# Performance work log

Measured on AMD Instinct MI355X. Metric: run time of the kernel, lower is better.

The kernel has to match this reference:

```python
import jax, jax.numpy as jnp
import numpy as np

N_NODES = 50000
N_EDGES = 600000
D = 128
H_MLP = 256
N_LABELS = 10
EPS = 0.0  # tf_geometric GIN default eps


def _gin_layer(x, src, dst, W, b):
    # gather neighbor (source) features and sum-aggregate into destinations
    msg = x[src]                                   # [E, D] irregular gather
    agg = jax.ops.segment_sum(msg, dst, num_segments=N_NODES)  # [N, D]
    h = (1.0 + EPS) * x + agg                      # GIN sum update
    return jax.nn.relu(h @ W + b)                  # dense transform + relu


def setup_inputs() -> dict:
    key = jax.random.key(0)
    ks = jax.random.split(key, 8)
    x = jax.random.normal(ks[0], (N_NODES, D), dtype=jnp.float32)
    edge_index = jax.random.randint(ks[1], (2, N_EDGES), 0, N_NODES, dtype=jnp.int32)
    s = 1.0 / np.sqrt(D)
    W0 = jax.random.normal(ks[2], (D, D), dtype=jnp.float32) * s
    W1 = jax.random.normal(ks[3], (D, D), dtype=jnp.float32) * s
    W2 = jax.random.normal(ks[4], (D, D), dtype=jnp.float32) * s
    Wm1 = jax.random.normal(ks[5], (D, H_MLP), dtype=jnp.float32) * s
    Wm2 = jax.random.normal(ks[6], (H_MLP, N_LABELS), dtype=jnp.float32) * (1.0 / np.sqrt(H_MLP))
    return {
        'x': x, 'edge_index': edge_index,
        'W0': W0, 'b0': jnp.zeros((D,), jnp.float32),
        'W1': W1, 'b1': jnp.zeros((D,), jnp.float32),
        'W2': W2, 'b2': jnp.zeros((D,), jnp.float32),
        'Wm1': Wm1, 'bm1': jnp.zeros((H_MLP,), jnp.float32),
        'Wm2': Wm2, 'bm2': jnp.zeros((N_LABELS,), jnp.float32),
    }


def reference(x, edge_index, W0, b0, W1, b1, W2, b2, Wm1, bm1, Wm2, bm2):
    src, dst = edge_index[0], edge_index[1]
    h = _gin_layer(x, src, dst, W0, b0)
    h = _gin_layer(h, src, dst, W1, b1)
    h = _gin_layer(h, src, dst, W2, b2)
    # head: Flatten is identity on [N, D]; Dense(256, relu) -> Dense(num_labels)
    h = jax.nn.relu(h @ Wm1 + bm1)
    return h @ Wm2 + bm2  # [N, num_labels] logits
```

## Files before the change

kernel.cpp:

```cpp
#include <hip/hip_runtime.h>


typedef short short8 __attribute__((ext_vector_type(8)));
typedef float v4f __attribute__((ext_vector_type(4)));
typedef float v2f __attribute__((ext_vector_type(2)));

#define BCAP 1024
#define MAXB 1024
#define NBIN 512

__device__ inline unsigned short f2bf(float f) {
  union { float f; unsigned int u; } c; c.f = f;
  unsigned int u = c.u;
  return (unsigned short)((u + 0x7fffu + ((u >> 16) & 1u)) >> 16);
}
__device__ inline float bfbits2f(unsigned int hi) {
  union { unsigned int u; float f; } c; c.u = hi; return c.f;
}
__device__ inline unsigned int pack2(float a, float b) {
  return (unsigned int)f2bf(a) | ((unsigned int)f2bf(b) << 16);
}
__device__ inline void add8(float* s, uint4 v) {
  s[0] += bfbits2f(v.x << 16); s[1] += bfbits2f(v.x & 0xffff0000u);
  s[2] += bfbits2f(v.y << 16); s[3] += bfbits2f(v.y & 0xffff0000u);
  s[4] += bfbits2f(v.z << 16); s[5] += bfbits2f(v.z & 0xffff0000u);
  s[6] += bfbits2f(v.w << 16); s[7] += bfbits2f(v.w & 0xffff0000u);
}
__device__ inline void addf8q(float* s, uint4 v) {
  v2f p;
  p = __builtin_amdgcn_cvt_pk_f32_fp8(v.x, false); s[0]  += p.x; s[1]  += p.y;
  p = __builtin_amdgcn_cvt_pk_f32_fp8(v.x, true);  s[2]  += p.x; s[3]  += p.y;
  p = __builtin_amdgcn_cvt_pk_f32_fp8(v.y, false); s[4]  += p.x; s[5]  += p.y;
  p = __builtin_amdgcn_cvt_pk_f32_fp8(v.y, true);  s[6]  += p.x; s[7]  += p.y;
  p = __builtin_amdgcn_cvt_pk_f32_fp8(v.z, false); s[8]  += p.x; s[9]  += p.y;
  p = __builtin_amdgcn_cvt_pk_f32_fp8(v.z, true);  s[10] += p.x; s[11] += p.y;
  p = __builtin_amdgcn_cvt_pk_f32_fp8(v.w, false); s[12] += p.x; s[13] += p.y;
  p = __builtin_amdgcn_cvt_pk_f32_fp8(v.w, true);  s[14] += p.x; s[15] += p.y;
}
__device__ inline unsigned char f2fp8(float v) {
  return (unsigned char)(__builtin_amdgcn_cvt_pk_fp8_f32(v, v, 0, false) & 0xff);
}
__device__ inline int wave_incl_scan_int(int v, int lane) {
#pragma unroll
  for (int off = 1; off < 64; off <<= 1) {
    int t = __shfl_up(v, off, 64);
    if (lane >= off) v += t;
  }
  return v;
}

__global__ __launch_bounds__(256) void prep_bin(
    const float* __restrict__ W0, const float* __restrict__ W1, const float* __restrict__ W2,
    const float* __restrict__ Wm1, const float* __restrict__ Wm2,
    unsigned short* __restrict__ W0T, unsigned short* __restrict__ W1T,
    unsigned short* __restrict__ W2T, unsigned short* __restrict__ Wm1T,
    unsigned short* __restrict__ Wm2T,
    const float* __restrict__ x, unsigned short* __restrict__ xb,
    unsigned char* __restrict__ xq, int n8, int PB,
    const int* __restrict__ src, const int* __restrict__ dst, int E, int per,
    int* __restrict__ bcnt, int* __restrict__ bucketA, int nbuckets) {
  __shared__ int hist[MAXB];
  __shared__ int base[MAXB];
  const int tid = threadIdx.x;
  if (blockIdx.x < PB) {
    int i = blockIdx.x * 256 + tid;
    if (i < n8) {
      const float4* p = (const float4*)x;
      float4 a = p[2 * (size_t)i], b = p[2 * (size_t)i + 1];
      uint4 o;
      o.x = pack2(a.x, a.y); o.y = pack2(a.z, a.w);
      o.z = pack2(b.x, b.y); o.w = pack2(b.z, b.w);
      ((uint4*)xb)[i] = o;
      unsigned int lo = 0, hi = 0;
      lo = __builtin_amdgcn_cvt_pk_fp8_f32(a.x, a.y, lo, false);
      lo = __builtin_amdgcn_cvt_pk_fp8_f32(a.z, a.w, lo, true);
      hi = __builtin_amdgcn_cvt_pk_fp8_f32(b.x, b.y, hi, false);
      hi = __builtin_amdgcn_cvt_pk_fp8_f32(b.z, b.w, hi, true);
      uint2 q; q.x = lo; q.y = hi;
      ((uint2*)xq)[i] = q;
    }
    if (i < 49152) {
      int w = i / 16384, r = i % 16384;
      int frag = r >> 9, l = (r >> 3) & 63, j = r & 7;
      int kq = frag >> 3, nfr = frag & 7;
      int nn = nfr * 16 + (l & 15);
      int k  = kq * 32 + (l >> 4) * 8 + j;
      const float* W = (w == 0) ? W0 : (w == 1) ? W1 : W2;
      unsigned short* O = (w == 0) ? W0T : (w == 1) ? W1T : W2T;
      O[r] = f2bf(W[k * 128 + nn]);
    } else if (i < 49152 + 32768) {
      int r = i - 49152;
      int frag = r >> 9, l = (r >> 3) & 63, j = r & 7;
      int kq = frag >> 4, nfr = frag & 15;
      int nn = nfr * 16 + (l & 15);
      int k  = kq * 32 + (l >> 4) * 8 + j;
      Wm1T[r] = f2bf(Wm1[k * 256 + nn]);
    } else if (i < 49152 + 32768 + 4096) {
      int r = i - 49152 - 32768;
      int kq = r >> 9, l = (r >> 3) & 63, j = r & 7;
      int nn = l & 15;
      int k  = kq * 32 + (l >> 4) * 8 + j;
      Wm2T[r] = (nn < 10) ? f2bf(Wm2[k * 10 + nn]) : (unsigned short)0;
    }
  } else {
    const int bb = blockIdx.x - PB;
    const int e0 = bb * per;
    const int e1 = (e0 + per < E) ? e0 + per : E;
    for (int j = tid; j < nbuckets; j += 256) hist[j] = 0;
    __syncthreads();
    for (int i = e0 + tid; i < e1; i += 256) atomicAdd(&hist[dst[i] >> 6], 1);
    __syncthreads();
    for (int j = tid; j < nbuckets; j += 256) {
      int h = hist[j];
      base[j] = h ? atomicAdd(&bcnt[j], h) : 0;
    }
    __syncthreads();
    for (int i = e0 + tid; i < e1; i += 256) {
      int d = dst[i], s = src[i];
      int b = d >> 6;
      int r = atomicAdd(&base[b], 1);
      bucketA[(size_t)b * BCAP + r] = (s << 6) | (d & 63);
    }
  }
}

__global__ __launch_bounds__(256) void fused_sort_layer(
    const unsigned short* __restrict__ Xb, const unsigned char* __restrict__ Xq,
    const int* __restrict__ bcnt, const int* __restrict__ bucketA,
    int* __restrict__ srcsS, int* __restrict__ boffs,
    const unsigned short* __restrict__ BT, const float* __restrict__ bias,
    unsigned char* __restrict__ Cq, int M) {
  __shared__ __align__(16) unsigned short As[64 * 136];
  __shared__ int rawE[BCAP];
  __shared__ int srcS[BCAP];
  __shared__ int hist[64], cur[64], offs[65];
  const int tid = threadIdx.x;
  const int lane = tid & 63;
  const int b = blockIdx.x;
  const int blk = b * 64;
  const int cnt = bcnt[b];

  for (int i = tid; i < cnt; i += 256) rawE[i] = bucketA[(size_t)b * BCAP + i];
  if (tid < 64) hist[tid] = 0;
  __syncthreads();
  for (int i = tid; i < cnt; i += 256) atomicAdd(&hist[rawE[i] & 63], 1);
  __syncthreads();
  if (tid < 64) {
    int v = hist[tid];
    int incl = wave_incl_scan_int(v, tid);
    offs[tid] = incl - v;
    cur[tid] = incl - v;
    if (tid == 63) offs[64] = incl;
  }
  __syncthreads();
  for (int i = tid; i < cnt; i += 256) {
    int e = rawE[i];
    int p = atomicAdd(&cur[e & 63], 1);
    int sv = e >> 6;
    srcS[p] = sv;
    srcsS[(size_t)b * BCAP + p] = sv;
  }
  if (tid < 65) boffs[b * 65 + tid] = offs[tid];
  __syncthreads();

  const int l = tid & 7, g = tid >> 3;
  const uint4* baseb = (const uint4*)Xb;
  const uint4* baseq = (const uint4*)Xq;
#pragma unroll
  for (int s2 = 0; s2 < 2; ++s2) {
    int nl = s2 * 32 + g;
    int node = blk + nl;
    float s[16] = {0, 0, 0, 0, 0, 0, 0, 0, 0, 0, 0, 0, 0, 0, 0, 0};
    if (node < M) {
      add8(s, baseb[(size_t)node * 16 + l * 2]);
      add8(s + 8, baseb[(size_t)node * 16 + l * 2 + 1]);
      int beg = offs[nl], c = offs[nl + 1] - beg;
      int j = 0;
      for (; j + 8 <= c; j += 8) {
        int i0 = srcS[beg + j + 0], i1 = srcS[beg + j + 1];
        int i2 = srcS[beg + j + 2], i3 = srcS[beg + j + 3];
        int i4 = srcS[beg + j + 4], i5 = srcS[beg + j + 5];
        int i6 = srcS[beg + j + 6], i7 = srcS[beg + j + 7];
        uint4 v0 = baseq[(size_t)i0 * 8 + l];
        uint4 v1 = baseq[(size_t)i1 * 8 + l];
        uint4 v2 = baseq[(size_t)i2 * 8 + l];
        uint4 v3 = baseq[(size_t)i3 * 8 + l];
        uint4 v4 = baseq[(size_t)i4 * 8 + l];
        uint4 v5 = baseq[(size_t)i5 * 8 + l];
        uint4 v6 = baseq[(size_t)i6 * 8 + l];
        uint4 v7 = baseq[(size_t)i7 * 8 + l];
        addf8q(s, v0); addf8q(s, v1); addf8q(s, v2); addf8q(s, v3);
        addf8q(s, v4); addf8q(s, v5); addf8q(s, v6); addf8q(s, v7);
      }
      if (j + 4 <= c) {
        int i0 = srcS[beg + j + 0], i1 = srcS[beg + j + 1];
        int i2 = srcS[beg + j + 2], i3 = srcS[beg + j + 3];
        uint4 v0 = baseq[(size_t)i0 * 8 + l];
        uint4 v1 = baseq[(size_t)i1 * 8 + l];
        uint4 v2 = baseq[(size_t)i2 * 8 + l];
        uint4 v3 = baseq[(size_t)i3 * 8 + l];
        addf8q(s, v0); addf8q(s, v1); addf8q(s, v2); addf8q(s, v3);
        j += 4;
      }
      if (j + 2 <= c) {
        int i0 = srcS[beg + j + 0], i1 = srcS[beg + j + 1];
        uint4 v0 = baseq[(size_t)i0 * 8 + l];
        uint4 v1 = baseq[(size_t)i1 * 8 + l];
        addf8q(s, v0); addf8q(s, v1);
        j += 2;
      }
      if (j < c) addf8q(s, baseq[(size_t)srcS[beg + j] * 8 + l]);
    }
    uint4 o0, o1;
    o0.x = pack2(s[0], s[1]);   o0.y = pack2(s[2], s[3]);
    o0.z = pack2(s[4], s[5]);   o0.w = pack2(s[6], s[7]);
    o1.x = pack2(s[8], s[9]);   o1.y = pack2(s[10], s[11]);
    o1.z = pack2(s[12], s[13]); o1.w = pack2(s[14], s[15]);
    *(uint4*)&As[nl * 136 + l * 16] = o0;
    *(uint4*)&As[nl * 136 + l * 16 + 8] = o1;
  }
  __syncthreads();

  const int w = tid >> 6;
  const int wm = w & 1, wn = w >> 1;
  const int l15 = lane & 15, quad = lane >> 4;
  const int mb = wm * 32, nb2 = wn * 64;

  v4f acc[2][4];
#pragma unroll
  for (int mf = 0; mf < 2; ++mf)
#pragma unroll
    for (int nf = 0; nf < 4; ++nf) acc[mf][nf] = (v4f)0.f;

#pragma unroll
  for (int k0 = 0; k0 < 128; k0 += 32) {
    const int kq = k0 >> 5;
    short8 a[2], bv[4];
#pragma unroll
    for (int mf = 0; mf < 2; ++mf)
      a[mf] = *(const short8*)&As[(mb + mf * 16 + l15) * 136 + k0 + quad * 8];
#pragma unroll
    for (int nf = 0; nf < 4; ++nf)
      bv[nf] = *(const short8*)(BT + (size_t)(kq * 8 + wn * 4 + nf) * 512 + lane * 8);
#pragma unroll
    for (int mf = 0; mf < 2; ++mf)
#pragma unroll
      for (int nf = 0; nf < 4; ++nf)
        acc[mf][nf] = __builtin_amdgcn_mfma_f32_16x16x32_bf16(a[mf], bv[nf], acc[mf][nf], 0, 0, 0);
  }
  __syncthreads();

  unsigned char* Cs = (unsigned char*)As;
#pragma unroll
  for (int mf = 0; mf < 2; ++mf)
#pragma unroll
    for (int r = 0; r < 4; ++r) {
      int row = mb + mf * 16 + quad * 4 + r;
#pragma unroll
      for (int nf = 0; nf < 4; ++nf) {
        int col = nb2 + nf * 16 + l15;
        Cs[row * 128 + col] = f2fp8(fmaxf(acc[mf][nf][r] + bias[col], 0.f));
      }
    }
  __syncthreads();
  uint4* dst4 = (uint4*)(Cq + (size_t)blk * 128);
  const uint4* s4 = (const uint4*)Cs;
  if (blk + 64 <= M) {
    dst4[tid] = s4[tid];
    dst4[tid + 256] = s4[tid + 256];
  } else {
    for (int c2 = tid; c2 < 512; c2 += 256)
      if (blk + (c2 >> 3) < M) dst4[c2] = s4[c2];
  }
}

__global__ __launch_bounds__(256) void fused_layer(
    const unsigned char* __restrict__ Xq,
    const int* __restrict__ bcnt,
    const int* __restrict__ srcsS, const int* __restrict__ boffs,
    const unsigned short* __restrict__ BT, const float* __restrict__ bias,
    unsigned char* __restrict__ Cq, int M) {
  __shared__ __align__(16) unsigned short As[64 * 136];
  __shared__ int srcS[BCAP];
  __shared__ int offs[65];
  const int tid = threadIdx.x;
  const int lane = tid & 63;
  const int b = blockIdx.x;
  const int blk = b * 64;
  const int cnt = bcnt[b];

  if (tid < 65) offs[tid] = boffs[b * 65 + tid];
  for (int i = tid; i < cnt; i += 256) srcS[i] = srcsS[(size_t)b * BCAP + i];
  __syncthreads();

  const int l = tid & 7, g = tid >> 3;
  const uint4* baseq = (const uint4*)Xq;
#pragma unroll
  for (int s2 = 0; s2 < 2; ++s2) {
    int nl = s2 * 32 + g;
    int node = blk + nl;
    float s[16] = {0, 0, 0, 0, 0, 0, 0, 0, 0, 0, 0, 0, 0, 0, 0, 0};
    if (node < M) {
      addf8q(s, baseq[(size_t)node * 8 + l]);
      int beg = offs[nl], c = offs[nl + 1] - beg;
      int j = 0;
      for (; j + 8 <= c; j += 8) {
        int i0 = srcS[beg + j + 0], i1 = srcS[beg + j + 1];
        int i2 = srcS[beg + j + 2], i3 = srcS[beg + j + 3];
        int i4 = srcS[beg + j + 4], i5 = srcS[beg + j + 5];
        int i6 = srcS[beg + j + 6], i7 = srcS[beg + j + 7];
        uint4 v0 = baseq[(size_t)i0 * 8 + l];
        uint4 v1 = baseq[(size_t)i1 * 8 + l];
        uint4 v2 = baseq[(size_t)i2 * 8 + l];
        uint4 v3 = baseq[(size_t)i3 * 8 + l];
        uint4 v4 = baseq[(size_t)i4 * 8 + l];
        uint4 v5 = baseq[(size_t)i5 * 8 + l];
        uint4 v6 = baseq[(size_t)i6 * 8 + l];
        uint4 v7 = baseq[(size_t)i7 * 8 + l];
        addf8q(s, v0); addf8q(s, v1); addf8q(s, v2); addf8q(s, v3);
        addf8q(s, v4); addf8q(s, v5); addf8q(s, v6); addf8q(s, v7);
      }
      if (j + 4 <= c) {
        int i0 = srcS[beg + j + 0], i1 = srcS[beg + j + 1];
        int i2 = srcS[beg + j + 2], i3 = srcS[beg + j + 3];
        uint4 v0 = baseq[(size_t)i0 * 8 + l];
        uint4 v1 = baseq[(size_t)i1 * 8 + l];
        uint4 v2 = baseq[(size_t)i2 * 8 + l];
        uint4 v3 = baseq[(size_t)i3 * 8 + l];
        addf8q(s, v0); addf8q(s, v1); addf8q(s, v2); addf8q(s, v3);
        j += 4;
      }
      if (j + 2 <= c) {
        int i0 = srcS[beg + j + 0], i1 = srcS[beg + j + 1];
        uint4 v0 = baseq[(size_t)i0 * 8 + l];
        uint4 v1 = baseq[(size_t)i1 * 8 + l];
        addf8q(s, v0); addf8q(s, v1);
        j += 2;
      }
      if (j < c) addf8q(s, baseq[(size_t)srcS[beg + j] * 8 + l]);
    }
    uint4 o0, o1;
    o0.x = pack2(s[0], s[1]);   o0.y = pack2(s[2], s[3]);
    o0.z = pack2(s[4], s[5]);   o0.w = pack2(s[6], s[7]);
    o1.x = pack2(s[8], s[9]);   o1.y = pack2(s[10], s[11]);
    o1.z = pack2(s[12], s[13]); o1.w = pack2(s[14], s[15]);
    *(uint4*)&As[nl * 136 + l * 16] = o0;
    *(uint4*)&As[nl * 136 + l * 16 + 8] = o1;
  }
  __syncthreads();

  const int w = tid >> 6;
  const int wm = w & 1, wn = w >> 1;
  const int l15 = lane & 15, quad = lane >> 4;
  const int mb = wm * 32, nb2 = wn * 64;

  v4f acc[2][4];
#pragma unroll
  for (int mf = 0; mf < 2; ++mf)
#pragma unroll
    for (int nf = 0; nf < 4; ++nf) acc[mf][nf] = (v4f)0.f;

#pragma unroll
  for (int k0 = 0; k0 < 128; k0 += 32) {
    const int kq = k0 >> 5;
    short8 a[2], bv[4];
#pragma unroll
    for (int mf = 0; mf < 2; ++mf)
      a[mf] = *(const short8*)&As[(mb + mf * 16 + l15) * 136 + k0 + quad * 8];
#pragma unroll
    for (int nf = 0; nf < 4; ++nf)
      bv[nf] = *(const short8*)(BT + (size_t)(kq * 8 + wn * 4 + nf) * 512 + lane * 8);
#pragma unroll
    for (int mf = 0; mf < 2; ++mf)
#pragma unroll
      for (int nf = 0; nf < 4; ++nf)
        acc[mf][nf] = __builtin_amdgcn_mfma_f32_16x16x32_bf16(a[mf], bv[nf], acc[mf][nf], 0, 0, 0);
  }
  __syncthreads();

  unsigned char* Cs = (unsigned char*)As;
#pragma unroll
  for (int mf = 0; mf < 2; ++mf)
#pragma unroll
    for (int r = 0; r < 4; ++r) {
      int row = mb + mf * 16 + quad * 4 + r;
#pragma unroll
      for (int nf = 0; nf < 4; ++nf) {
        int col = nb2 + nf * 16 + l15;
        Cs[row * 128 + col] = f2fp8(fmaxf(acc[mf][nf][r] + bias[col], 0.f));
      }
    }
  __syncthreads();
  uint4* dst4 = (uint4*)(Cq + (size_t)blk * 128);
  const uint4* s4 = (const uint4*)Cs;
  if (blk + 64 <= M) {
    dst4[tid] = s4[tid];
    dst4[tid + 256] = s4[tid + 256];
  } else {
    for (int c2 = tid; c2 < 512; c2 += 256)
      if (blk + (c2 >> 3) < M) dst4[c2] = s4[c2];
  }
}

__global__ __launch_bounds__(256) void fused_l3_head(
    const unsigned char* __restrict__ Xq,
    const int* __restrict__ bcnt,
    const int* __restrict__ srcsS, const int* __restrict__ boffs,
    const unsigned short* __restrict__ W2T, const float* __restrict__ b2,
    const unsigned short* __restrict__ Wm1T, const float* __restrict__ bm1,
    const unsigned short* __restrict__ Wm2T, const float* __restrict__ bm2,
    float* __restrict__ out, int M, int NOUT) {
  __shared__ __align__(16) unsigned char lds[64 * 264 * 2];
  unsigned short* As = (unsigned short*)lds;
  int* srcS = (int*)(lds + 64 * 136 * 2);
  unsigned short* Hs = (unsigned short*)lds;
  __shared__ int offs[65];
  const int tid = threadIdx.x;
  const int lane = tid & 63;
  const int b = blockIdx.x;
  const int blk = b * 64;
  const int cnt = bcnt[b];

  if (tid < 65) offs[tid] = boffs[b * 65 + tid];
  for (int i = tid; i < cnt; i += 256) srcS[i] = srcsS[(size_t)b * BCAP + i];
  __syncthreads();

  const int l = tid & 7, g = tid >> 3;
  const uint4* baseq = (const uint4*)Xq;
#pragma unroll
  for (int s2 = 0; s2 < 2; ++s2) {
    int nl = s2 * 32 + g;
    int node = blk + nl;
    float s[16] = {0, 0, 0, 0, 0, 0, 0, 0, 0, 0, 0, 0, 0, 0, 0, 0};
    if (node < M) {
      addf8q(s, baseq[(size_t)node * 8 + l]);
      int beg = offs[nl], c = offs[nl + 1] - beg;
      int j = 0;
      for (; j + 8 <= c; j += 8) {
        int i0 = srcS[beg + j + 0], i1 = srcS[beg + j + 1];
        int i2 = srcS[beg + j + 2], i3 = srcS[beg + j + 3];
        int i4 = srcS[beg + j + 4], i5 = srcS[beg + j + 5];
        int i6 = srcS[beg + j + 6], i7 = srcS[beg + j + 7];
        uint4 v0 = baseq[(size_t)i0 * 8 + l];
        uint4 v1 = baseq[(size_t)i1 * 8 + l];
        uint4 v2 = baseq[(size_t)i2 * 8 + l];
        uint4 v3 = baseq[(size_t)i3 * 8 + l];
        uint4 v4 = baseq[(size_t)i4 * 8 + l];
        uint4 v5 = baseq[(size_t)i5 * 8 + l];
        uint4 v6 = baseq[(size_t)i6 * 8 + l];
        uint4 v7 = baseq[(size_t)i7 * 8 + l];
        addf8q(s, v0); addf8q(s, v1); addf8q(s, v2); addf8q(s, v3);
        addf8q(s, v4); addf8q(s, v5); addf8q(s, v6); addf8q(s, v7);
      }
      if (j + 4 <= c) {
        int i0 = srcS[beg + j + 0], i1 = srcS[beg + j + 1];
        int i2 = srcS[beg + j + 2], i3 = srcS[beg + j + 3];
        uint4 v0 = baseq[(size_t)i0 * 8 + l];
        uint4 v1 = baseq[(size_t)i1 * 8 + l];
        uint4 v2 = baseq[(size_t)i2 * 8 + l];
        uint4 v3 = baseq[(size_t)i3 * 8 + l];
        addf8q(s, v0); addf8q(s, v1); addf8q(s, v2); addf8q(s, v3);
        j += 4;
      }
      if (j + 2 <= c) {
        int i0 = srcS[beg + j + 0], i1 = srcS[beg + j + 1];
        uint4 v0 = baseq[(size_t)i0 * 8 + l];
        uint4 v1 = baseq[(size_t)i1 * 8 + l];
        addf8q(s, v0); addf8q(s, v1);
        j += 2;
      }
      if (j < c) addf8q(s, baseq[(size_t)srcS[beg + j] * 8 + l]);
    }
    uint4 o0, o1;
    o0.x = pack2(s[0], s[1]);   o0.y = pack2(s[2], s[3]);
    o0.z = pack2(s[4], s[5]);   o0.w = pack2(s[6], s[7]);
    o1.x = pack2(s[8], s[9]);   o1.y = pack2(s[10], s[11]);
    o1.z = pack2(s[12], s[13]); o1.w = pack2(s[14], s[15]);
    *(uint4*)&As[nl * 136 + l * 16] = o0;
    *(uint4*)&As[nl * 136 + l * 16 + 8] = o1;
  }
  __syncthreads();

  const int w = tid >> 6;
  const int wm = w & 1, wn = w >> 1;
  const int l15 = lane & 15, quad = lane >> 4;
  const int mb = wm * 32, nb2 = wn * 64;

  v4f acc[2][4];
#pragma unroll
  for (int mf = 0; mf < 2; ++mf)
#pragma unroll
    for (int nf = 0; nf < 4; ++nf) acc[mf][nf] = (v4f)0.f;

#pragma unroll
  for (int k0 = 0; k0 < 128; k0 += 32) {
    const int kq = k0 >> 5;
    short8 a[2], bv[4];
#pragma unroll
    for (int mf = 0; mf < 2; ++mf)
      a[mf] = *(const short8*)&As[(mb + mf * 16 + l15) * 136 + k0 + quad * 8];
#pragma unroll
    for (int nf = 0; nf < 4; ++nf)
      bv[nf] = *(const short8*)(W2T + (size_t)(kq * 8 + wn * 4 + nf) * 512 + lane * 8);
#pragma unroll
    for (int mf = 0; mf < 2; ++mf)
#pragma unroll
      for (int nf = 0; nf < 4; ++nf)
        acc[mf][nf] = __builtin_amdgcn_mfma_f32_16x16x32_bf16(a[mf], bv[nf], acc[mf][nf], 0, 0, 0);
  }
  __syncthreads();

#pragma unroll
  for (int mf = 0; mf < 2; ++mf)
#pragma unroll
    for (int r = 0; r < 4; ++r) {
      int row = mb + mf * 16 + quad * 4 + r;
#pragma unroll
      for (int nf = 0; nf < 4; ++nf) {
        int col = nb2 + nf * 16 + l15;
        As[row * 136 + col] = f2bf(fmaxf(acc[mf][nf][r] + b2[col], 0.f));
      }
    }
  __syncthreads();

  const int nbH = wn * 128;
  v4f acc2[2][8];
#pragma unroll
  for (int mf = 0; mf < 2; ++mf)
#pragma unroll
    for (int nf = 0; nf < 8; ++nf) acc2[mf][nf] = (v4f)0.f;

#pragma unroll
  for (int k0 = 0; k0 < 128; k0 += 32) {
    const int kq = k0 >> 5;
    short8 a[2];
#pragma unroll
    for (int mf = 0; mf < 2; ++mf)
      a[mf] = *(const short8*)&As[(mb + mf * 16 + l15) * 136 + k0 + quad * 8];
#pragma unroll
    for (int nf = 0; nf < 8; ++nf) {
      short8 bb = *(const short8*)(Wm1T + (size_t)(kq * 16 + wn * 8 + nf) * 512 + lane * 8);
#pragma unroll
      for (int mf = 0; mf < 2; ++mf)
        acc2[mf][nf] = __builtin_amdgcn_mfma_f32_16x16x32_bf16(a[mf], bb, acc2[mf][nf], 0, 0, 0);
    }
  }
  __syncthreads();

#pragma unroll
  for (int mf = 0; mf < 2; ++mf)
#pragma unroll
    for (int r = 0; r < 4; ++r) {
      int row = mb + mf * 16 + quad * 4 + r;
#pragma unroll
      for (int nf = 0; nf < 8; ++nf) {
        int col = nbH + nf * 16 + l15;
        Hs[row * 264 + col] = f2bf(fmaxf(acc2[mf][nf][r] + bm1[col], 0.f));
      }
    }
  __syncthreads();

  const int rowl = w * 16 + l15;
  v4f acc3 = (v4f)0.f;
#pragma unroll
  for (int k0 = 0; k0 < 256; k0 += 32)
    acc3 = __builtin_amdgcn_mfma_f32_16x16x32_bf16(
        *(const short8*)&Hs[rowl * 264 + k0 + quad * 8],
        *(const short8*)(Wm2T + (size_t)(k0 >> 5) * 512 + lane * 8), acc3, 0, 0, 0);
  float bb = (l15 < NOUT) ? bm2[l15] : 0.f;
#pragma unroll
  for (int r = 0; r < 4; ++r) {
    int grow = blk + w * 16 + quad * 4 + r;
    if (grow < M && l15 < NOUT) out[(size_t)grow * NOUT + l15] = acc3[r] + bb;
  }
}


extern "C" void kernel_launch(void* const* d_in, const int* in_sizes, int n_in,
                              void* d_out, int out_size, void* d_ws, size_t ws_size,
                              hipStream_t stream) {
  const float* x   = (const float*)d_in[0];
  const int*   ei  = (const int*)d_in[1];
  const float* W0  = (const float*)d_in[2];
  const float* b0  = (const float*)d_in[3];
  const float* W1  = (const float*)d_in[4];
  const float* b1  = (const float*)d_in[5];
  const float* W2  = (const float*)d_in[6];
  const float* b2  = (const float*)d_in[7];
  const float* Wm1 = (const float*)d_in[8];
  const float* bm1 = (const float*)d_in[9];
  const float* Wm2 = (const float*)d_in[10];
  const float* bm2 = (const float*)d_in[11];
  float* out = (float*)d_out;

  const int D = 128;
  const int N = in_sizes[0] / D;
  const int E = in_sizes[1] / 2;
  const int L = in_sizes[11];
  const int nb = (N + 63) / 64;

  const int* srcv = ei;
  const int* dstv = ei + E;

  char* ws = (char*)d_ws;
  size_t off = 0;
  auto alloc = [&](size_t bytes) -> void* {
    void* p = ws + off;
    off = (off + bytes + 255) & ~(size_t)255;
    return p;
  };
  int* bcnt    = (int*)alloc((size_t)MAXB * 4);
  int* bucketA = (int*)alloc((size_t)nb * BCAP * 4);
  int* srcsS   = (int*)alloc((size_t)nb * BCAP * 4);
  int* boffs   = (int*)alloc((size_t)nb * 65 * 4);
  unsigned short* xb   = (unsigned short*)alloc((size_t)N * 128 * 2);
  unsigned char*  xq   = (unsigned char*)alloc((size_t)N * 128);
  unsigned char*  h1q  = (unsigned char*)alloc((size_t)N * 128);
  unsigned char*  h2q  = (unsigned char*)alloc((size_t)N * 128);
  unsigned short* W0T  = (unsigned short*)alloc(128 * 128 * 2);
  unsigned short* W1T  = (unsigned short*)alloc(128 * 128 * 2);
  unsigned short* W2T  = (unsigned short*)alloc(128 * 128 * 2);
  unsigned short* Wm1T = (unsigned short*)alloc(256 * 128 * 2);
  unsigned short* Wm2T = (unsigned short*)alloc(16 * 256 * 2);
  (void)ws_size; (void)n_in; (void)out_size;

  const int tpb = 256;
  int n8 = N * 16;
  const int PB = (n8 + tpb - 1) / tpb;
  int per = (E + NBIN - 1) / NBIN;

  hipMemsetAsync(bcnt, 0, (size_t)MAXB * 4, stream);
  prep_bin<<<dim3(PB + NBIN), dim3(tpb), 0, stream>>>(
      W0, W1, W2, Wm1, Wm2, W0T, W1T, W2T, Wm1T, Wm2T,
      x, xb, xq, n8, PB, srcv, dstv, E, per, bcnt, bucketA, nb);

  dim3 lgrid(nb);
  fused_sort_layer<<<lgrid, dim3(tpb), 0, stream>>>(
      xb, xq, bcnt, bucketA, srcsS, boffs, W0T, b0, h1q, N);
  fused_layer<<<lgrid, dim3(tpb), 0, stream>>>(
      h1q, bcnt, srcsS, boffs, W1T, b1, h2q, N);
  fused_l3_head<<<lgrid, dim3(tpb), 0, stream>>>(
      h2q, bcnt, srcsS, boffs, W2T, b2, Wm1T, bm1, Wm2T, bm2, out, N, L);
}
```

Before: 198.6 us.

## Convert fused GIN layer kernels to persistent blocks with atomic tile scheduling

The three fused layer kernels now launch a fixed grid of 512 blocks. Each block repeatedly takes the next 64-node tile from a global atomic counter instead of mapping one tile to each block. The intent is to balance the irregular per-tile edge counts dynamically and to cut block launch overhead across the 782 tiles. In exchange it adds an atomic and two barriers per tile, and it relies on the memset covering the counters placed right after bcnt.

```diff
diff --git a/kernel.cpp b/kernel.cpp
--- a/kernel.cpp
+++ b/kernel.cpp
@@ -8,6 +8,7 @@
 #define BCAP 1024
 #define MAXB 1024
 #define NBIN 512
+#define LGRID 512
 
 __device__ inline unsigned short f2bf(float f) {
   union { float f; unsigned int u; } c; c.f = f;
@@ -129,148 +130,156 @@
     const int* __restrict__ bcnt, const int* __restrict__ bucketA,
     int* __restrict__ srcsS, int* __restrict__ boffs,
     const unsigned short* __restrict__ BT, const float* __restrict__ bias,
-    unsigned char* __restrict__ Cq, int M) {
+    unsigned char* __restrict__ Cq, int M, int nb, int* __restrict__ ctr) {
   __shared__ __align__(16) unsigned short As[64 * 136];
   __shared__ int rawE[BCAP];
   __shared__ int srcS[BCAP];
   __shared__ int hist[64], cur[64], offs[65];
+  __shared__ int sb;
   const int tid = threadIdx.x;
   const int lane = tid & 63;
-  const int b = blockIdx.x;
-  const int blk = b * 64;
-  const int cnt = bcnt[b];
-
-  for (int i = tid; i < cnt; i += 256) rawE[i] = bucketA[(size_t)b * BCAP + i];
-  if (tid < 64) hist[tid] = 0;
-  __syncthreads();
-  for (int i = tid; i < cnt; i += 256) atomicAdd(&hist[rawE[i] & 63], 1);
-  __syncthreads();
-  if (tid < 64) {
-    int v = hist[tid];
-    int incl = wave_incl_scan_int(v, tid);
-    offs[tid] = incl - v;
-    cur[tid] = incl - v;
-    if (tid == 63) offs[64] = incl;
-  }
-  __syncthreads();
-  for (int i = tid; i < cnt; i += 256) {
-    int e = rawE[i];
-    int p = atomicAdd(&cur[e & 63], 1);
-    int sv = e >> 6;
-    srcS[p] = sv;
-    srcsS[(size_t)b * BCAP + p] = sv;
-  }
-  if (tid < 65) boffs[b * 65 + tid] = offs[tid];
-  __syncthreads();
-
-  const int l = tid & 7, g = tid >> 3;
-  const uint4* baseb = (const uint4*)Xb;
-  const uint4* baseq = (const uint4*)Xq;
-#pragma unroll
-  for (int s2 = 0; s2 < 2; ++s2) {
-    int nl = s2 * 32 + g;
-    int node = blk + nl;
-    float s[16] = {0, 0, 0, 0, 0, 0, 0, 0, 0, 0, 0, 0, 0, 0, 0, 0};
-    if (node < M) {
-      add8(s, baseb[(size_t)node * 16 + l * 2]);
-      add8(s + 8, baseb[(size_t)node * 16 + l * 2 + 1]);
-      int beg = offs[nl], c = offs[nl + 1] - beg;
-      int j = 0;
-      for (; j + 8 <= c; j += 8) {
-        int i0 = srcS[beg + j + 0], i1 = srcS[beg + j + 1];
-        int i2 = srcS[beg + j + 2], i3 = srcS[beg + j + 3];
-        int i4 = srcS[beg + j + 4], i5 = srcS[beg + j + 5];
-        int i6 = srcS[beg + j + 6], i7 = srcS[beg + j + 7];
-        uint4 v0 = baseq[(size_t)i0 * 8 + l];
-        uint4 v1 = baseq[(size_t)i1 * 8 + l];
-        uint4 v2 = baseq[(size_t)i2 * 8 + l];
-        uint4 v3 = baseq[(size_t)i3 * 8 + l];
-        uint4 v4 = baseq[(size_t)i4 * 8 + l];
-        uint4 v5 = baseq[(size_t)i5 * 8 + l];
-        uint4 v6 = baseq[(size_t)i6 * 8 + l];
-        uint4 v7 = baseq[(size_t)i7 * 8 + l];
-        addf8q(s, v0); addf8q(s, v1); addf8q(s, v2); addf8q(s, v3);
-        addf8q(s, v4); addf8q(s, v5); addf8q(s, v6); addf8q(s, v7);
-      }
-      if (j + 4 <= c) {
-        int i0 = srcS[beg + j + 0], i1 = srcS[beg + j + 1];
-        int i2 = srcS[beg + j + 2], i3 = srcS[beg + j + 3];
-        uint4 v0 = baseq[(size_t)i0 * 8 + l];
-        uint4 v1 = baseq[(size_t)i1 * 8 + l];
-        uint4 v2 = baseq[(size_t)i2 * 8 + l];
-        uint4 v3 = baseq[(size_t)i3 * 8 + l];
-        addf8q(s, v0); addf8q(s, v1); addf8q(s, v2); addf8q(s, v3);
-        j += 4;
-      }
-      if (j + 2 <= c) {
-        int i0 = srcS[beg + j + 0], i1 = srcS[beg + j + 1];
-        uint4 v0 = baseq[(size_t)i0 * 8 + l];
-        uint4 v1 = baseq[(size_t)i1 * 8 + l];
-        addf8q(s, v0); addf8q(s, v1);
-        j += 2;
-      }
-      if (j < c) addf8q(s, baseq[(size_t)srcS[beg + j] * 8 + l]);
-    }
-    uint4 o0, o1;
-    o0.x = pack2(s[0], s[1]);   o0.y = pack2(s[2], s[3]);
-    o0.z = pack2(s[4], s[5]);   o0.w = pack2(s[6], s[7]);
-    o1.x = pack2(s[8], s[9]);   o1.y = pack2(s[10], s[11]);
-    o1.z = pack2(s[12], s[13]); o1.w = pack2(s[14], s[15]);
-    *(uint4*)&As[nl * 136 + l * 16] = o0;
-    *(uint4*)&As[nl * 136 + l * 16 + 8] = o1;
-  }
-  __syncthreads();
-
-  const int w = tid >> 6;
-  const int wm = w & 1, wn = w >> 1;
-  const int l15 = lane & 15, quad = lane >> 4;
-  const int mb = wm * 32, nb2 = wn * 64;
-
-  v4f acc[2][4];
-#pragma unroll
-  for (int mf = 0; mf < 2; ++mf)
-#pragma unroll
-    for (int nf = 0; nf < 4; ++nf) acc[mf][nf] = (v4f)0.f;
-
-#pragma unroll
-  for (int k0 = 0; k0 < 128; k0 += 32) {
-    const int kq = k0 >> 5;
-    short8 a[2], bv[4];
-#pragma unroll
-    for (int mf = 0; mf < 2; ++mf)
-      a[mf] = *(const short8*)&As[(mb + mf * 16 + l15) * 136 + k0 + quad * 8];
-#pragma unroll
-    for (int nf = 0; nf < 4; ++nf)
-      bv[nf] = *(const short8*)(BT + (size_t)(kq * 8 + wn * 4 + nf) * 512 + lane * 8);
-#pragma unroll
-    for (int mf = 0; mf < 2; ++mf)
+
+  for (;;) {
+    __syncthreads();
+    if (tid == 0) sb = atomicAdd(ctr, 1);
+    __syncthreads();
+    const int b = sb;
+    if (b >= nb) break;
+    const int blk = b * 64;
+    const int cnt = bcnt[b];
+
+    for (int i = tid; i < cnt; i += 256) rawE[i] = bucketA[(size_t)b * BCAP + i];
+    if (tid < 64) hist[tid] = 0;
+    __syncthreads();
+    for (int i = tid; i < cnt; i += 256) atomicAdd(&hist[rawE[i] & 63], 1);
+    __syncthreads();
+    if (tid < 64) {
+      int v = hist[tid];
+      int incl = wave_incl_scan_int(v, tid);
+      offs[tid] = incl - v;
+      cur[tid] = incl - v;
+      if (tid == 63) offs[64] = incl;
+    }
+    __syncthreads();
+    for (int i = tid; i < cnt; i += 256) {
+      int e = rawE[i];
+      int p = atomicAdd(&cur[e & 63], 1);
+      int sv = e >> 6;
+      srcS[p] = sv;
+      srcsS[(size_t)b * BCAP + p] = sv;
+    }
+    if (tid < 65) boffs[b * 65 + tid] = offs[tid];
+    __syncthreads();
+
+    const int l = tid & 7, g = tid >> 3;
+    const uint4* baseb = (const uint4*)Xb;
+    const uint4* baseq = (const uint4*)Xq;
+#pragma unroll
+    for (int s2 = 0; s2 < 2; ++s2) {
+      int nl = s2 * 32 + g;
+      int node = blk + nl;
+      float s[16] = {0, 0, 0, 0, 0, 0, 0, 0, 0, 0, 0, 0, 0, 0, 0, 0};
+      if (node < M) {
+        add8(s, baseb[(size_t)node * 16 + l * 2]);
+        add8(s + 8, baseb[(size_t)node * 16 + l * 2 + 1]);
+        int beg = offs[nl], c = offs[nl + 1] - beg;
+        int j = 0;
+        for (; j + 8 <= c; j += 8) {
+          int i0 = srcS[beg + j + 0], i1 = srcS[beg + j + 1];
+          int i2 = srcS[beg + j + 2], i3 = srcS[beg + j + 3];
+          int i4 = srcS[beg + j + 4], i5 = srcS[beg + j + 5];
+          int i6 = srcS[beg + j + 6], i7 = srcS[beg + j + 7];
+          uint4 v0 = baseq[(size_t)i0 * 8 + l];
+          uint4 v1 = baseq[(size_t)i1 * 8 + l];
+          uint4 v2 = baseq[(size_t)i2 * 8 + l];
+          uint4 v3 = baseq[(size_t)i3 * 8 + l];
+          uint4 v4 = baseq[(size_t)i4 * 8 + l];
+          uint4 v5 = baseq[(size_t)i5 * 8 + l];
+          uint4 v6 = baseq[(size_t)i6 * 8 + l];
+          uint4 v7 = baseq[(size_t)i7 * 8 + l];
+          addf8q(s, v0); addf8q(s, v1); addf8q(s, v2); addf8q(s, v3);
+          addf8q(s, v4); addf8q(s, v5); addf8q(s, v6); addf8q(s, v7);
+        }
+        if (j + 4 <= c) {
+          int i0 = srcS[beg + j + 0], i1 = srcS[beg + j + 1];
+          int i2 = srcS[beg + j + 2], i3 = srcS[beg + j + 3];
+          uint4 v0 = baseq[(size_t)i0 * 8 + l];
+          uint4 v1 = baseq[(size_t)i1 * 8 + l];
+          uint4 v2 = baseq[(size_t)i2 * 8 + l];
+          uint4 v3 = baseq[(size_t)i3 * 8 + l];
+          addf8q(s, v0); addf8q(s, v1); addf8q(s, v2); addf8q(s, v3);
+          j += 4;
+        }
+        if (j + 2 <= c) {
+          int i0 = srcS[beg + j + 0], i1 = srcS[beg + j + 1];
+          uint4 v0 = baseq[(size_t)i0 * 8 + l];
+          uint4 v1 = baseq[(size_t)i1 * 8 + l];
+          addf8q(s, v0); addf8q(s, v1);
+          j += 2;
+        }
+        if (j < c) addf8q(s, baseq[(size_t)srcS[beg + j] * 8 + l]);
+      }
+      uint4 o0, o1;
+      o0.x = pack2(s[0], s[1]);   o0.y = pack2(s[2], s[3]);
+      o0.z = pack2(s[4], s[5]);   o0.w = pack2(s[6], s[7]);
+      o1.x = pack2(s[8], s[9]);   o1.y = pack2(s[10], s[11]);
+      o1.z = pack2(s[12], s[13]); o1.w = pack2(s[14], s[15]);
+      *(uint4*)&As[nl * 136 + l * 16] = o0;
+      *(uint4*)&As[nl * 136 + l * 16 + 8] = o1;
+    }
+    __syncthreads();
+
+    const int w = tid >> 6;
+    const int wm = w & 1, wn = w >> 1;
+    const int l15 = lane & 15, quad = lane >> 4;
+    const int mb = wm * 32, nb2 = wn * 64;
+
+    v4f acc[2][4];
+#pragma unroll
+    for (int mf = 0; mf < 2; ++mf)
+#pragma unroll
+      for (int nf = 0; nf < 4; ++nf) acc[mf][nf] = (v4f)0.f;
+
+#pragma unroll
+    for (int k0 = 0; k0 < 128; k0 += 32) {
+      const int kq = k0 >> 5;
+      short8 a[2], bv[4];
+#pragma unroll
+      for (int mf = 0; mf < 2; ++mf)
+        a[mf] = *(const short8*)&As[(mb + mf * 16 + l15) * 136 + k0 + quad * 8];
 #pragma unroll
       for (int nf = 0; nf < 4; ++nf)
-        acc[mf][nf] = __builtin_amdgcn_mfma_f32_16x16x32_bf16(a[mf], bv[nf], acc[mf][nf], 0, 0, 0);
-  }
-  __syncthreads();
-
-  unsigned char* Cs = (unsigned char*)As;
-#pragma unroll
-  for (int mf = 0; mf < 2; ++mf)
-#pragma unroll
-    for (int r = 0; r < 4; ++r) {
-      int row = mb + mf * 16 + quad * 4 + r;
-#pragma unroll
-      for (int nf = 0; nf < 4; ++nf) {
-        int col = nb2 + nf * 16 + l15;
-        Cs[row * 128 + col] = f2fp8(fmaxf(acc[mf][nf][r] + bias[col], 0.f));
-      }
-    }
-  __syncthreads();
-  uint4* dst4 = (uint4*)(Cq + (size_t)blk * 128);
-  const uint4* s4 = (const uint4*)Cs;
-  if (blk + 64 <= M) {
-    dst4[tid] = s4[tid];
-    dst4[tid + 256] = s4[tid + 256];
-  } else {
-    for (int c2 = tid; c2 < 512; c2 += 256)
-      if (blk + (c2 >> 3) < M) dst4[c2] = s4[c2];
+        bv[nf] = *(const short8*)(BT + (size_t)(kq * 8 + wn * 4 + nf) * 512 + lane * 8);
+#pragma unroll
+      for (int mf = 0; mf < 2; ++mf)
+#pragma unroll
+        for (int nf = 0; nf < 4; ++nf)
+          acc[mf][nf] = __builtin_amdgcn_mfma_f32_16x16x32_bf16(a[mf], bv[nf], acc[mf][nf], 0, 0, 0);
+    }
+    __syncthreads();
+
+    unsigned char* Cs = (unsigned char*)As;
+#pragma unroll
+    for (int mf = 0; mf < 2; ++mf)
+#pragma unroll
+      for (int r = 0; r < 4; ++r) {
+        int row = mb + mf * 16 + quad * 4 + r;
+#pragma unroll
+        for (int nf = 0; nf < 4; ++nf) {
+          int col = nb2 + nf * 16 + l15;
+          Cs[row * 128 + col] = f2fp8(fmaxf(acc[mf][nf][r] + bias[col], 0.f));
+        }
+      }
+    __syncthreads();
+    uint4* dst4 = (uint4*)(Cq + (size_t)blk * 128);
+    const uint4* s4 = (const uint4*)Cs;
+    if (blk + 64 <= M) {
+      dst4[tid] = s4[tid];
+      dst4[tid + 256] = s4[tid + 256];
+    } else {
+      for (int c2 = tid; c2 < 512; c2 += 256)
+        if (blk + (c2 >> 3) < M) dst4[c2] = s4[c2];
+    }
   }
 }
 
@@ -279,126 +288,134 @@
     const int* __restrict__ bcnt,
     const int* __restrict__ srcsS, const int* __restrict__ boffs,
     const unsigned short* __restrict__ BT, const float* __restrict__ bias,
-    unsigned char* __restrict__ Cq, int M) {
+    unsigned char* __restrict__ Cq, int M, int nb, int* __restrict__ ctr) {
   __shared__ __align__(16) unsigned short As[64 * 136];
   __shared__ int srcS[BCAP];
   __shared__ int offs[65];
+  __shared__ int sb;
   const int tid = threadIdx.x;
   const int lane = tid & 63;
-  const int b = blockIdx.x;
-  const int blk = b * 64;
-  const int cnt = bcnt[b];
-
-  if (tid < 65) offs[tid] = boffs[b * 65 + tid];
-  for (int i = tid; i < cnt; i += 256) srcS[i] = srcsS[(size_t)b * BCAP + i];
-  __syncthreads();
-
-  const int l = tid & 7, g = tid >> 3;
-  const uint4* baseq = (const uint4*)Xq;
-#pragma unroll
-  for (int s2 = 0; s2 < 2; ++s2) {
-    int nl = s2 * 32 + g;
-    int node = blk + nl;
-    float s[16] = {0, 0, 0, 0, 0, 0, 0, 0, 0, 0, 0, 0, 0, 0, 0, 0};
-    if (node < M) {
-      addf8q(s, baseq[(size_t)node * 8 + l]);
-      int beg = offs[nl], c = offs[nl + 1] - beg;
-      int j = 0;
-      for (; j + 8 <= c; j += 8) {
-        int i0 = srcS[beg + j + 0], i1 = srcS[beg + j + 1];
-        int i2 = srcS[beg + j + 2], i3 = srcS[beg + j + 3];
-        int i4 = srcS[beg + j + 4], i5 = srcS[beg + j + 5];
-        int i6 = srcS[beg + j + 6], i7 = srcS[beg + j + 7];
-        uint4 v0 = baseq[(size_t)i0 * 8 + l];
-        uint4 v1 = baseq[(size_t)i1 * 8 + l];
-        uint4 v2 = baseq[(size_t)i2 * 8 + l];
-        uint4 v3 = baseq[(size_t)i3 * 8 + l];
-        uint4 v4 = baseq[(size_t)i4 * 8 + l];
-        uint4 v5 = baseq[(size_t)i5 * 8 + l];
-        uint4 v6 = baseq[(size_t)i6 * 8 + l];
-        uint4 v7 = baseq[(size_t)i7 * 8 + l];
-        addf8q(s, v0); addf8q(s, v1); addf8q(s, v2); addf8q(s, v3);
-        addf8q(s, v4); addf8q(s, v5); addf8q(s, v6); addf8q(s, v7);
-      }
-      if (j + 4 <= c) {
-        int i0 = srcS[beg + j + 0], i1 = srcS[beg + j + 1];
-        int i2 = srcS[beg + j + 2], i3 = srcS[beg + j + 3];
-        uint4 v0 = baseq[(size_t)i0 * 8 + l];
-        uint4 v1 = baseq[(size_t)i1 * 8 + l];
-        uint4 v2 = baseq[(size_t)i2 * 8 + l];
-        uint4 v3 = baseq[(size_t)i3 * 8 + l];
-        addf8q(s, v0); addf8q(s, v1); addf8q(s, v2); addf8q(s, v3);
-        j += 4;
-      }
-      if (j + 2 <= c) {
-        int i0 = srcS[beg + j + 0], i1 = srcS[beg + j + 1];
-        uint4 v0 = baseq[(size_t)i0 * 8 + l];
-        uint4 v1 = baseq[(size_t)i1 * 8 + l];
-        addf8q(s, v0); addf8q(s, v1);
-        j += 2;
-      }
-      if (j < c) addf8q(s, baseq[(size_t)srcS[beg + j] * 8 + l]);
-    }
-    uint4 o0, o1;
-    o0.x = pack2(s[0], s[1]);   o0.y = pack2(s[2], s[3]);
-    o0.z = pack2(s[4], s[5]);   o0.w = pack2(s[6], s[7]);
-    o1.x = pack2(s[8], s[9]);   o1.y = pack2(s[10], s[11]);
-    o1.z = pack2(s[12], s[13]); o1.w = pack2(s[14], s[15]);
-    *(uint4*)&As[nl * 136 + l * 16] = o0;
-    *(uint4*)&As[nl * 136 + l * 16 + 8] = o1;
-  }
-  __syncthreads();
-
-  const int w = tid >> 6;
-  const int wm = w & 1, wn = w >> 1;
-  const int l15 = lane & 15, quad = lane >> 4;
-  const int mb = wm * 32, nb2 = wn * 64;
-
-  v4f acc[2][4];
-#pragma unroll
-  for (int mf = 0; mf < 2; ++mf)
-#pragma unroll
-    for (int nf = 0; nf < 4; ++nf) acc[mf][nf] = (v4f)0.f;
-
-#pragma unroll
-  for (int k0 = 0; k0 < 128; k0 += 32) {
-    const int kq = k0 >> 5;
-    short8 a[2], bv[4];
-#pragma unroll
-    for (int mf = 0; mf < 2; ++mf)
-      a[mf] = *(const short8*)&As[(mb + mf * 16 + l15) * 136 + k0 + quad * 8];
-#pragma unroll
-    for (int nf = 0; nf < 4; ++nf)
-      bv[nf] = *(const short8*)(BT + (size_t)(kq * 8 + wn * 4 + nf) * 512 + lane * 8);
-#pragma unroll
-    for (int mf = 0; mf < 2; ++mf)
+
+  for (;;) {
+    __syncthreads();
+    if (tid == 0) sb = atomicAdd(ctr, 1);
+    __syncthreads();
+    const int b = sb;
+    if (b >= nb) break;
+    const int blk = b * 64;
+    const int cnt = bcnt[b];
+
+    if (tid < 65) offs[tid] = boffs[b * 65 + tid];
+    for (int i = tid; i < cnt; i += 256) srcS[i] = srcsS[(size_t)b * BCAP + i];
+    __syncthreads();
+
+    const int l = tid & 7, g = tid >> 3;
+    const uint4* baseq = (const uint4*)Xq;
+#pragma unroll
+    for (int s2 = 0; s2 < 2; ++s2) {
+      int nl = s2 * 32 + g;
+      int node = blk + nl;
+      float s[16] = {0, 0, 0, 0, 0, 0, 0, 0, 0, 0, 0, 0, 0, 0, 0, 0};
+      if (node < M) {
+        addf8q(s, baseq[(size_t)node * 8 + l]);
+        int beg = offs[nl], c = offs[nl + 1] - beg;
+        int j = 0;
+        for (; j + 8 <= c; j += 8) {
+          int i0 = srcS[beg + j + 0], i1 = srcS[beg + j + 1];
+          int i2 = srcS[beg + j + 2], i3 = srcS[beg + j + 3];
+          int i4 = srcS[beg + j + 4], i5 = srcS[beg + j + 5];
+          int i6 = srcS[beg + j + 6], i7 = srcS[beg + j + 7];
+          uint4 v0 = baseq[(size_t)i0 * 8 + l];
+          uint4 v1 = baseq[(size_t)i1 * 8 + l];
+          uint4 v2 = baseq[(size_t)i2 * 8 + l];
+          uint4 v3 = baseq[(size_t)i3 * 8 + l];
+          uint4 v4 = baseq[(size_t)i4 * 8 + l];
+          uint4 v5 = baseq[(size_t)i5 * 8 + l];
+          uint4 v6 = baseq[(size_t)i6 * 8 + l];
+          uint4 v7 = baseq[(size_t)i7 * 8 + l];
+          addf8q(s, v0); addf8q(s, v1); addf8q(s, v2); addf8q(s, v3);
+          addf8q(s, v4); addf8q(s, v5); addf8q(s, v6); addf8q(s, v7);
+        }
+        if (j + 4 <= c) {
+          int i0 = srcS[beg + j + 0], i1 = srcS[beg + j + 1];
+          int i2 = srcS[beg + j + 2], i3 = srcS[beg + j + 3];
+          uint4 v0 = baseq[(size_t)i0 * 8 + l];
+          uint4 v1 = baseq[(size_t)i1 * 8 + l];
+          uint4 v2 = baseq[(size_t)i2 * 8 + l];
+          uint4 v3 = baseq[(size_t)i3 * 8 + l];
+          addf8q(s, v0); addf8q(s, v1); addf8q(s, v2); addf8q(s, v3);
+          j += 4;
+        }
+        if (j + 2 <= c) {
+          int i0 = srcS[beg + j + 0], i1 = srcS[beg + j + 1];
+          uint4 v0 = baseq[(size_t)i0 * 8 + l];
+          uint4 v1 = baseq[(size_t)i1 * 8 + l];
+          addf8q(s, v0); addf8q(s, v1);
+          j += 2;
+        }
+        if (j < c) addf8q(s, baseq[(size_t)srcS[beg + j] * 8 + l]);
+      }
+      uint4 o0, o1;
+      o0.x = pack2(s[0], s[1]);   o0.y = pack2(s[2], s[3]);
+      o0.z = pack2(s[4], s[5]);   o0.w = pack2(s[6], s[7]);
+      o1.x = pack2(s[8], s[9]);   o1.y = pack2(s[10], s[11]);
+      o1.z = pack2(s[12], s[13]); o1.w = pack2(s[14], s[15]);
+      *(uint4*)&As[nl * 136 + l * 16] = o0;
+      *(uint4*)&As[nl * 136 + l * 16 + 8] = o1;
+    }
+    __syncthreads();
+
+    const int w = tid >> 6;
+    const int wm = w & 1, wn = w >> 1;
+    const int l15 = lane & 15, quad = lane >> 4;
+    const int mb = wm * 32, nb2 = wn * 64;
+
+    v4f acc[2][4];
+#pragma unroll
+    for (int mf = 0; mf < 2; ++mf)
+#pragma unroll
+      for (int nf = 0; nf < 4; ++nf) acc[mf][nf] = (v4f)0.f;
+
+#pragma unroll
+    for (int k0 = 0; k0 < 128; k0 += 32) {
+      const int kq = k0 >> 5;
+      short8 a[2], bv[4];
+#pragma unroll
+      for (int mf = 0; mf < 2; ++mf)
+        a[mf] = *(const short8*)&As[(mb + mf * 16 + l15) * 136 + k0 + quad * 8];
 #pragma unroll
       for (int nf = 0; nf < 4; ++nf)
-        acc[mf][nf] = __builtin_amdgcn_mfma_f32_16x16x32_bf16(a[mf], bv[nf], acc[mf][nf], 0, 0, 0);
-  }
-  __syncthreads();
-
-  unsigned char* Cs = (unsigned char*)As;
-#pragma unroll
-  for (int mf = 0; mf < 2; ++mf)
-#pragma unroll
-    for (int r = 0; r < 4; ++r) {
-      int row = mb + mf * 16 + quad * 4 + r;
-#pragma unroll
-      for (int nf = 0; nf < 4; ++nf) {
-        int col = nb2 + nf * 16 + l15;
-        Cs[row * 128 + col] = f2fp8(fmaxf(acc[mf][nf][r] + bias[col], 0.f));
-      }
-    }
-  __syncthreads();
-  uint4* dst4 = (uint4*)(Cq + (size_t)blk * 128);
-  const uint4* s4 = (const uint4*)Cs;
-  if (blk + 64 <= M) {
-    dst4[tid] = s4[tid];
-    dst4[tid + 256] = s4[tid + 256];
-  } else {
-    for (int c2 = tid; c2 < 512; c2 += 256)
-      if (blk + (c2 >> 3) < M) dst4[c2] = s4[c2];
+        bv[nf] = *(const short8*)(BT + (size_t)(kq * 8 + wn * 4 + nf) * 512 + lane * 8);
+#pragma unroll
+      for (int mf = 0; mf < 2; ++mf)
+#pragma unroll
+        for (int nf = 0; nf < 4; ++nf)
+          acc[mf][nf] = __builtin_amdgcn_mfma_f32_16x16x32_bf16(a[mf], bv[nf], acc[mf][nf], 0, 0, 0);
+    }
+    __syncthreads();
+
+    unsigned char* Cs = (unsigned char*)As;
+#pragma unroll
+    for (int mf = 0; mf < 2; ++mf)
+#pragma unroll
+      for (int r = 0; r < 4; ++r) {
+        int row = mb + mf * 16 + quad * 4 + r;
+#pragma unroll
+        for (int nf = 0; nf < 4; ++nf) {
+          int col = nb2 + nf * 16 + l15;
+          Cs[row * 128 + col] = f2fp8(fmaxf(acc[mf][nf][r] + bias[col], 0.f));
+        }
+      }
+    __syncthreads();
+    uint4* dst4 = (uint4*)(Cq + (size_t)blk * 128);
+    const uint4* s4 = (const uint4*)Cs;
+    if (blk + 64 <= M) {
+      dst4[tid] = s4[tid];
+      dst4[tid + 256] = s4[tid + 256];
+    } else {
+      for (int c2 = tid; c2 < 512; c2 += 256)
+        if (blk + (c2 >> 3) < M) dst4[c2] = s4[c2];
+    }
   }
 }
 
@@ -409,169 +426,177 @@
     const unsigned short* __restrict__ W2T, const float* __restrict__ b2,
     const unsigned short* __restrict__ Wm1T, const float* __restrict__ bm1,
     const unsigned short* __restrict__ Wm2T, const float* __restrict__ bm2,
-    float* __restrict__ out, int M, int NOUT) {
+    float* __restrict__ out, int M, int NOUT, int nb, int* __restrict__ ctr) {
   __shared__ __align__(16) unsigned char lds[64 * 264 * 2];
   unsigned short* As = (unsigned short*)lds;
   int* srcS = (int*)(lds + 64 * 136 * 2);
   unsigned short* Hs = (unsigned short*)lds;
   __shared__ int offs[65];
+  __shared__ int sb;
   const int tid = threadIdx.x;
   const int lane = tid & 63;
-  const int b = blockIdx.x;
-  const int blk = b * 64;
-  const int cnt = bcnt[b];
-
-  if (tid < 65) offs[tid] = boffs[b * 65 + tid];
-  for (int i = tid; i < cnt; i += 256) srcS[i] = srcsS[(size_t)b * BCAP + i];
-  __syncthreads();
-
-  const int l = tid & 7, g = tid >> 3;
-  const uint4* baseq = (const uint4*)Xq;
-#pragma unroll
-  for (int s2 = 0; s2 < 2; ++s2) {
-    int nl = s2 * 32 + g;
-    int node = blk + nl;
-    float s[16] = {0, 0, 0, 0, 0, 0, 0, 0, 0, 0, 0, 0, 0, 0, 0, 0};
-    if (node < M) {
-      addf8q(s, baseq[(size_t)node * 8 + l]);
-      int beg = offs[nl], c = offs[nl + 1] - beg;
-      int j = 0;
-      for (; j + 8 <= c; j += 8) {
-        int i0 = srcS[beg + j + 0], i1 = srcS[beg + j + 1];
-        int i2 = srcS[beg + j + 2], i3 = srcS[beg + j + 3];
-        int i4 = srcS[beg + j + 4], i5 = srcS[beg + j + 5];
-        int i6 = srcS[beg + j + 6], i7 = srcS[beg + j + 7];
-        uint4 v0 = baseq[(size_t)i0 * 8 + l];
-        uint4 v1 = baseq[(size_t)i1 * 8 + l];
-        uint4 v2 = baseq[(size_t)i2 * 8 + l];
-        uint4 v3 = baseq[(size_t)i3 * 8 + l];
-        uint4 v4 = baseq[(size_t)i4 * 8 + l];
-        uint4 v5 = baseq[(size_t)i5 * 8 + l];
-        uint4 v6 = baseq[(size_t)i6 * 8 + l];
-        uint4 v7 = baseq[(size_t)i7 * 8 + l];
-        addf8q(s, v0); addf8q(s, v1); addf8q(s, v2); addf8q(s, v3);
-        addf8q(s, v4); addf8q(s, v5); addf8q(s, v6); addf8q(s, v7);
-      }
-      if (j + 4 <= c) {
-        int i0 = srcS[beg + j + 0], i1 = srcS[beg + j + 1];
-        int i2 = srcS[beg + j + 2], i3 = srcS[beg + j + 3];
-        uint4 v0 = baseq[(size_t)i0 * 8 + l];
-        uint4 v1 = baseq[(size_t)i1 * 8 + l];
-        uint4 v2 = baseq[(size_t)i2 * 8 + l];
-        uint4 v3 = baseq[(size_t)i3 * 8 + l];
-        addf8q(s, v0); addf8q(s, v1); addf8q(s, v2); addf8q(s, v3);
-        j += 4;
-      }
-      if (j + 2 <= c) {
-        int i0 = srcS[beg + j + 0], i1 = srcS[beg + j + 1];
-        uint4 v0 = baseq[(size_t)i0 * 8 + l];
-        uint4 v1 = baseq[(size_t)i1 * 8 + l];
-        addf8q(s, v0); addf8q(s, v1);
-        j += 2;
-      }
-      if (j < c) addf8q(s, baseq[(size_t)srcS[beg + j] * 8 + l]);
-    }
-    uint4 o0, o1;
-    o0.x = pack2(s[0], s[1]);   o0.y = pack2(s[2], s[3]);
-    o0.z = pack2(s[4], s[5]);   o0.w = pack2(s[6], s[7]);
-    o1.x = pack2(s[8], s[9]);   o1.y = pack2(s[10], s[11]);
-    o1.z = pack2(s[12], s[13]); o1.w = pack2(s[14], s[15]);
-    *(uint4*)&As[nl * 136 + l * 16] = o0;
-    *(uint4*)&As[nl * 136 + l * 16 + 8] = o1;
-  }
-  __syncthreads();
-
-  const int w = tid >> 6;
-  const int wm = w & 1, wn = w >> 1;
-  const int l15 = lane & 15, quad = lane >> 4;
-  const int mb = wm * 32, nb2 = wn * 64;
-
-  v4f acc[2][4];
-#pragma unroll
-  for (int mf = 0; mf < 2; ++mf)
-#pragma unroll
-    for (int nf = 0; nf < 4; ++nf) acc[mf][nf] = (v4f)0.f;
-
-#pragma unroll
-  for (int k0 = 0; k0 < 128; k0 += 32) {
-    const int kq = k0 >> 5;
-    short8 a[2], bv[4];
-#pragma unroll
-    for (int mf = 0; mf < 2; ++mf)
-      a[mf] = *(const short8*)&As[(mb + mf * 16 + l15) * 136 + k0 + quad * 8];
-#pragma unroll
-    for (int nf = 0; nf < 4; ++nf)
-      bv[nf] = *(const short8*)(W2T + (size_t)(kq * 8 + wn * 4 + nf) * 512 + lane * 8);
-#pragma unroll
-    for (int mf = 0; mf < 2; ++mf)
+
+  for (;;) {
+    __syncthreads();
+    if (tid == 0) sb = atomicAdd(ctr, 1);
+    __syncthreads();
+    const int b = sb;
+    if (b >= nb) break;
+    const int blk = b * 64;
+    const int cnt = bcnt[b];
+
+    if (tid < 65) offs[tid] = boffs[b * 65 + tid];
+    for (int i = tid; i < cnt; i += 256) srcS[i] = srcsS[(size_t)b * BCAP + i];
+    __syncthreads();
+
+    const int l = tid & 7, g = tid >> 3;
+    const uint4* baseq = (const uint4*)Xq;
+#pragma unroll
+    for (int s2 = 0; s2 < 2; ++s2) {
+      int nl = s2 * 32 + g;
+      int node = blk + nl;
+      float s[16] = {0, 0, 0, 0, 0, 0, 0, 0, 0, 0, 0, 0, 0, 0, 0, 0};
+      if (node < M) {
+        addf8q(s, baseq[(size_t)node * 8 + l]);
+        int beg = offs[nl], c = offs[nl + 1] - beg;
+        int j = 0;
+        for (; j + 8 <= c; j += 8) {
+          int i0 = srcS[beg + j + 0], i1 = srcS[beg + j + 1];
+          int i2 = srcS[beg + j + 2], i3 = srcS[beg + j + 3];
+          int i4 = srcS[beg + j + 4], i5 = srcS[beg + j + 5];
+          int i6 = srcS[beg + j + 6], i7 = srcS[beg + j + 7];
+          uint4 v0 = baseq[(size_t)i0 * 8 + l];
+          uint4 v1 = baseq[(size_t)i1 * 8 + l];
+          uint4 v2 = baseq[(size_t)i2 * 8 + l];
+          uint4 v3 = baseq[(size_t)i3 * 8 + l];
+          uint4 v4 = baseq[(size_t)i4 * 8 + l];
+          uint4 v5 = baseq[(size_t)i5 * 8 + l];
+          uint4 v6 = baseq[(size_t)i6 * 8 + l];
+          uint4 v7 = baseq[(size_t)i7 * 8 + l];
+          addf8q(s, v0); addf8q(s, v1); addf8q(s, v2); addf8q(s, v3);
+          addf8q(s, v4); addf8q(s, v5); addf8q(s, v6); addf8q(s, v7);
+        }
+        if (j + 4 <= c) {
+          int i0 = srcS[beg + j + 0], i1 = srcS[beg + j + 1];
+          int i2 = srcS[beg + j + 2], i3 = srcS[beg + j + 3];
+          uint4 v0 = baseq[(size_t)i0 * 8 + l];
+          uint4 v1 = baseq[(size_t)i1 * 8 + l];
+          uint4 v2 = baseq[(size_t)i2 * 8 + l];
+          uint4 v3 = baseq[(size_t)i3 * 8 + l];
+          addf8q(s, v0); addf8q(s, v1); addf8q(s, v2); addf8q(s, v3);
+          j += 4;
+        }
+        if (j + 2 <= c) {
+          int i0 = srcS[beg + j + 0], i1 = srcS[beg + j + 1];
+          uint4 v0 = baseq[(size_t)i0 * 8 + l];
+          uint4 v1 = baseq[(size_t)i1 * 8 + l];
+          addf8q(s, v0); addf8q(s, v1);
+          j += 2;
+        }
+        if (j < c) addf8q(s, baseq[(size_t)srcS[beg + j] * 8 + l]);
+      }
+      uint4 o0, o1;
+      o0.x = pack2(s[0], s[1]);   o0.y = pack2(s[2], s[3]);
+      o0.z = pack2(s[4], s[5]);   o0.w = pack2(s[6], s[7]);
+      o1.x = pack2(s[8], s[9]);   o1.y = pack2(s[10], s[11]);
+      o1.z = pack2(s[12], s[13]); o1.w = pack2(s[14], s[15]);
+      *(uint4*)&As[nl * 136 + l * 16] = o0;
+      *(uint4*)&As[nl * 136 + l * 16 + 8] = o1;
+    }
+    __syncthreads();
+
+    const int w = tid >> 6;
+    const int wm = w & 1, wn = w >> 1;
+    const int l15 = lane & 15, quad = lane >> 4;
+    const int mb = wm * 32, nb2 = wn * 64;
+
+    v4f acc[2][4];
+#pragma unroll
+    for (int mf = 0; mf < 2; ++mf)
+#pragma unroll
+      for (int nf = 0; nf < 4; ++nf) acc[mf][nf] = (v4f)0.f;
+
+#pragma unroll
+    for (int k0 = 0; k0 < 128; k0 += 32) {
+      const int kq = k0 >> 5;
+      short8 a[2], bv[4];
+#pragma unroll
+      for (int mf = 0; mf < 2; ++mf)
+        a[mf] = *(const short8*)&As[(mb + mf * 16 + l15) * 136 + k0 + quad * 8];
 #pragma unroll
       for (int nf = 0; nf < 4; ++nf)
-        acc[mf][nf] = __builtin_amdgcn_mfma_f32_16x16x32_bf16(a[mf], bv[nf], acc[mf][nf], 0, 0, 0);
-  }
-  __syncthreads();
-
-#pragma unroll
-  for (int mf = 0; mf < 2; ++mf)
+        bv[nf] = *(const short8*)(W2T + (size_t)(kq * 8 + wn * 4 + nf) * 512 + lane * 8);
+#pragma unroll
+      for (int mf = 0; mf < 2; ++mf)
+#pragma unroll
+        for (int nf = 0; nf < 4; ++nf)
+          acc[mf][nf] = __builtin_amdgcn_mfma_f32_16x16x32_bf16(a[mf], bv[nf], acc[mf][nf], 0, 0, 0);
+    }
+    __syncthreads();
+
+#pragma unroll
+    for (int mf = 0; mf < 2; ++mf)
+#pragma unroll
+      for (int r = 0; r < 4; ++r) {
+        int row = mb + mf * 16 + quad * 4 + r;
+#pragma unroll
+        for (int nf = 0; nf < 4; ++nf) {
+          int col = nb2 + nf * 16 + l15;
+          As[row * 136 + col] = f2bf(fmaxf(acc[mf][nf][r] + b2[col], 0.f));
+        }
+      }
+    __syncthreads();
+
+    const int nbH = wn * 128;
+    v4f acc2[2][8];
+#pragma unroll
+    for (int mf = 0; mf < 2; ++mf)
+#pragma unroll
+      for (int nf = 0; nf < 8; ++nf) acc2[mf][nf] = (v4f)0.f;
+
+#pragma unroll
+    for (int k0 = 0; k0 < 128; k0 += 32) {
+      const int kq = k0 >> 5;
+      short8 a[2];
+#pragma unroll
+      for (int mf = 0; mf < 2; ++mf)
+        a[mf] = *(const short8*)&As[(mb + mf * 16 + l15) * 136 + k0 + quad * 8];
+#pragma unroll
+      for (int nf = 0; nf < 8; ++nf) {
+        short8 bb = *(const short8*)(Wm1T + (size_t)(kq * 16 + wn * 8 + nf) * 512 + lane * 8);
+#pragma unroll
+        for (int mf = 0; mf < 2; ++mf)
+          acc2[mf][nf] = __builtin_amdgcn_mfma_f32_16x16x32_bf16(a[mf], bb, acc2[mf][nf], 0, 0, 0);
+      }
+    }
+    __syncthreads();
+
+#pragma unroll
+    for (int mf = 0; mf < 2; ++mf)
+#pragma unroll
+      for (int r = 0; r < 4; ++r) {
+        int row = mb + mf * 16 + quad * 4 + r;
+#pragma unroll
+        for (int nf = 0; nf < 8; ++nf) {
+          int col = nbH + nf * 16 + l15;
+          Hs[row * 264 + col] = f2bf(fmaxf(acc2[mf][nf][r] + bm1[col], 0.f));
+        }
+      }
+    __syncthreads();
+
+    const int rowl = w * 16 + l15;
+    v4f acc3 = (v4f)0.f;
+#pragma unroll
+    for (int k0 = 0; k0 < 256; k0 += 32)
+      acc3 = __builtin_amdgcn_mfma_f32_16x16x32_bf16(
+          *(const short8*)&Hs[rowl * 264 + k0 + quad * 8],
+          *(const short8*)(Wm2T + (size_t)(k0 >> 5) * 512 + lane * 8), acc3, 0, 0, 0);
+    float bb = (l15 < NOUT) ? bm2[l15] : 0.f;
 #pragma unroll
     for (int r = 0; r < 4; ++r) {
-      int row = mb + mf * 16 + quad * 4 + r;
-#pragma unroll
-      for (int nf = 0; nf < 4; ++nf) {
-        int col = nb2 + nf * 16 + l15;
-        As[row * 136 + col] = f2bf(fmaxf(acc[mf][nf][r] + b2[col], 0.f));
-      }
-    }
-  __syncthreads();
-
-  const int nbH = wn * 128;
-  v4f acc2[2][8];
-#pragma unroll
-  for (int mf = 0; mf < 2; ++mf)
-#pragma unroll
-    for (int nf = 0; nf < 8; ++nf) acc2[mf][nf] = (v4f)0.f;
-
-#pragma unroll
-  for (int k0 = 0; k0 < 128; k0 += 32) {
-    const int kq = k0 >> 5;
-    short8 a[2];
-#pragma unroll
-    for (int mf = 0; mf < 2; ++mf)
-      a[mf] = *(const short8*)&As[(mb + mf * 16 + l15) * 136 + k0 + quad * 8];
-#pragma unroll
-    for (int nf = 0; nf < 8; ++nf) {
-      short8 bb = *(const short8*)(Wm1T + (size_t)(kq * 16 + wn * 8 + nf) * 512 + lane * 8);
-#pragma unroll
-      for (int mf = 0; mf < 2; ++mf)
-        acc2[mf][nf] = __builtin_amdgcn_mfma_f32_16x16x32_bf16(a[mf], bb, acc2[mf][nf], 0, 0, 0);
-    }
-  }
-  __syncthreads();
-
-#pragma unroll
-  for (int mf = 0; mf < 2; ++mf)
-#pragma unroll
-    for (int r = 0; r < 4; ++r) {
-      int row = mb + mf * 16 + quad * 4 + r;
-#pragma unroll
-      for (int nf = 0; nf < 8; ++nf) {
-        int col = nbH + nf * 16 + l15;
-        Hs[row * 264 + col] = f2bf(fmaxf(acc2[mf][nf][r] + bm1[col], 0.f));
-      }
-    }
-  __syncthreads();
-
-  const int rowl = w * 16 + l15;
-  v4f acc3 = (v4f)0.f;
-#pragma unroll
-  for (int k0 = 0; k0 < 256; k0 += 32)
-    acc3 = __builtin_amdgcn_mfma_f32_16x16x32_bf16(
-        *(const short8*)&Hs[rowl * 264 + k0 + quad * 8],
-        *(const short8*)(Wm2T + (size_t)(k0 >> 5) * 512 + lane * 8), acc3, 0, 0, 0);
-  float bb = (l15 < NOUT) ? bm2[l15] : 0.f;
-#pragma unroll
-  for (int r = 0; r < 4; ++r) {
-    int grow = blk + w * 16 + quad * 4 + r;
-    if (grow < M && l15 < NOUT) out[(size_t)grow * NOUT + l15] = acc3[r] + bb;
+      int grow = blk + w * 16 + quad * 4 + r;
+      if (grow < M && l15 < NOUT) out[(size_t)grow * NOUT + l15] = acc3[r] + bb;
+    }
   }
 }
 
@@ -610,6 +635,7 @@
     return p;
   };
   int* bcnt    = (int*)alloc((size_t)MAXB * 4);
+  int* ctrs    = (int*)alloc(256);
   int* bucketA = (int*)alloc((size_t)nb * BCAP * 4);
   int* srcsS   = (int*)alloc((size_t)nb * BCAP * 4);
   int* boffs   = (int*)alloc((size_t)nb * 65 * 4);
@@ -629,16 +655,17 @@
   const int PB = (n8 + tpb - 1) / tpb;
   int per = (E + NBIN - 1) / NBIN;
 
-  hipMemsetAsync(bcnt, 0, (size_t)MAXB * 4, stream);
+  hipMemsetAsync(bcnt, 0, (size_t)MAXB * 4 + 256, stream);
   prep_bin<<<dim3(PB + NBIN), dim3(tpb), 0, stream>>>(
       W0, W1, W2, Wm1, Wm2, W0T, W1T, W2T, Wm1T, Wm2T,
       x, xb, xq, n8, PB, srcv, dstv, E, per, bcnt, bucketA, nb);
 
-  dim3 lgrid(nb);
+  dim3 lgrid(LGRID);
   fused_sort_layer<<<lgrid, dim3(tpb), 0, stream>>>(
-      xb, xq, bcnt, bucketA, srcsS, boffs, W0T, b0, h1q, N);
+      xb, xq, bcnt, bucketA, srcsS, boffs, W0T, b0, h1q, N, nb, ctrs + 0);
   fused_layer<<<lgrid, dim3(tpb), 0, stream>>>(
-      h1q, bcnt, srcsS, boffs, W1T, b1, h2q, N);
+      h1q, bcnt, srcsS, boffs, W1T, b1, h2q, N, nb, ctrs + 16);
   fused_l3_head<<<lgrid, dim3(tpb), 0, stream>>>(
-      h2q, bcnt, srcsS, boffs, W2T, b2, Wm1T, bm1, Wm2T, bm2, out, N, L);
-}
+      h2q, bcnt, srcsS, boffs, W2T, b2, Wm1T, bm1, Wm2T, bm2, out, N, L,
+      nb, ctrs + 32);
+}
```

Measured after the change: 236.5 us. 1.19x slower.
